# Performance work log

Hardware: AMD Instinct MI355X
Metric: run time of the kernel (lower is better)

Reference implementation:

```python
import jax, jax.numpy as jnp
import numpy as np

B, T, K, DH = 64, 1024, 8, 256
H = 2 * DH  # gru hidden_size = 512


def setup_inputs() -> dict:
    key = jax.random.key(0)
    ks = jax.random.split(key, 8)
    scale = 1.0 / np.sqrt(H)
    return {
        "s": jax.random.normal(ks[0], (B, T, 1, DH), dtype=jnp.float32),
        "p": jax.random.normal(ks[1], (B, T, K, DH), dtype=jnp.float32),
        "W_ih": jax.random.uniform(ks[2], (3 * H, H), jnp.float32, -scale, scale),
        "W_hh": jax.random.uniform(ks[3], (3 * H, H), jnp.float32, -scale, scale),
        "b_ih": jax.random.uniform(ks[4], (3 * H,), jnp.float32, -scale, scale),
        "b_hh": jax.random.uniform(ks[5], (3 * H,), jnp.float32, -scale, scale),
        "W_t": jax.random.uniform(ks[6], (1, H), jnp.float32, -scale, scale),
        "b_t": jax.random.uniform(ks[7], (1,), jnp.float32, -scale, scale),
    }


def reference(s, p, W_ih, W_hh, b_ih, b_hh, W_t, b_t):
    # p is summed over its multi-hot dim, then concatenated with s -> GRU input.
    x = jnp.concatenate([s[:, :, 0, :], p.sum(axis=2)], axis=-1)  # [B, T, H]
    x = jnp.swapaxes(x, 0, 1)  # [T, B, H] (scan over time)
    # Precompute all input-side gate pre-activations in one big GEMM.
    gi = jnp.einsum("tbh,gh->tbg", x, W_ih) + b_ih  # [T, B, 3H]
    h0 = jnp.zeros((B, H), dtype=x.dtype)  # hidden reset per example (initHidden)

    def step(h, gi_t):
        gh = h @ W_hh.T + b_hh  # [B, 3H]
        i_r, i_z, i_n = jnp.split(gi_t, 3, axis=-1)
        h_r, h_z, h_n = jnp.split(gh, 3, axis=-1)
        r = jax.nn.sigmoid(i_r + h_r)
        z = jax.nn.sigmoid(i_z + h_z)
        n = jnp.tanh(i_n + r * h_n)
        h_new = (1.0 - z) * n + z * h
        return h_new, h_new

    _, hs = jax.lax.scan(step, h0, gi)  # hs: [T, B, H]
    # reward = sigmoid(Linear(hidden)) at every timestep
    rewards = jax.nn.sigmoid(jnp.einsum("tbh,oh->tbo", hs, W_t) + b_t)  # [T, B, 1]
    return jnp.swapaxes(rewards[..., 0], 0, 1)  # [B, T]
```

## Files before the change

kernel.cpp:

```cpp
#include <hip/hip_runtime.h>
#include <hip/hip_fp16.h>
#include <stdint.h>

#define TT 1024
#define BB 64
#define DHH 256
#define HH 512
#define G3 1536
#define CHK 256

typedef _Float16 f16;
typedef _Float16 f16x4 __attribute__((ext_vector_type(4)));
typedef _Float16 f16x8 __attribute__((ext_vector_type(8)));
typedef float f32x4 __attribute__((ext_vector_type(4)));
typedef unsigned long long u64;

__device__ __forceinline__ float sigm(float x){ return 1.0f/(1.0f+__expf(-x)); }
__device__ __forceinline__ float tanh_f(float x){ return 2.0f/(1.0f+__expf(-2.0f*x)) - 1.0f; }

__global__ void k_prep(const float* __restrict__ wih, const float* __restrict__ whh,
                       const float* __restrict__ bih, const float* __restrict__ bhh,
                       f16* __restrict__ wih_h, f16* __restrict__ whh_h, float* __restrict__ biasf){
  int i = blockIdx.x*256 + threadIdx.x;
  if (i < G3*HH){ wih_h[i] = (f16)wih[i]; whh_h[i] = (f16)whh[i]; }
  if (i < G3) biasf[i] = bih[i] + (i < 2*HH ? bhh[i] : 0.0f);
}

__global__ void k_buildx(const float* __restrict__ s, const float* __restrict__ p, f16* __restrict__ x){
  int m = blockIdx.x;
  int t = m >> 6, b = m & 63;
  int l = threadIdx.x;
  const float4* s4 = reinterpret_cast<const float4*>(s + ((size_t)b*TT + t)*DHH);
  const float4* p4 = reinterpret_cast<const float4*>(p + ((size_t)b*TT + t)*8*DHH);
  float4 sv = s4[l];
  float4 a  = p4[l];
#pragma unroll
  for (int k=1;k<8;k++){ float4 v = p4[k*64 + l]; a.x+=v.x; a.y+=v.y; a.z+=v.z; a.w+=v.w; }
  f16* xr = x + (size_t)m*HH;
  f16x4 hs = { (f16)sv.x,(f16)sv.y,(f16)sv.z,(f16)sv.w };
  f16x4 hp = { (f16)a.x,(f16)a.y,(f16)a.z,(f16)a.w };
  *reinterpret_cast<f16x4*>(xr + l*4)       = hs;
  *reinterpret_cast<f16x4*>(xr + 256 + l*4) = hp;
}

#define LDAP 72
__global__ __launch_bounds__(256) void k_gemm(const f16* __restrict__ x, const f16* __restrict__ w,
                       const float* __restrict__ biasf, f16* __restrict__ gi){
  __shared__ f16 lA[128*LDAP];
  __shared__ f16 lB[128*LDAP];
  int by = blockIdx.x;
  int bx = blockIdx.y;
  int tid = threadIdx.x, l = tid & 63, wv = tid >> 6;
  int wm = wv >> 1, wn = wv & 1;

  f32x4 acc[4][4];
#pragma unroll
  for (int i=0;i<4;i++)
#pragma unroll
    for (int j=0;j<4;j++) acc[i][j] = (f32x4){0.f,0.f,0.f,0.f};

  for (int kt = 0; kt < 8; ++kt){
#pragma unroll
    for (int r = 0; r < 4; ++r){
      int c = tid + 256*r;
      int row = c >> 3, o = c & 7;
      f16x8 va = *reinterpret_cast<const f16x8*>(w + (size_t)(by*128+row)*HH + kt*64 + o*8);
      f16x8 vb = *reinterpret_cast<const f16x8*>(x + (size_t)(bx*128+row)*HH + kt*64 + o*8);
      *reinterpret_cast<f16x8*>(&lA[row*LDAP + o*8]) = va;
      *reinterpret_cast<f16x8*>(&lB[row*LDAP + o*8]) = vb;
    }
    __syncthreads();
#pragma unroll
    for (int kk = 0; kk < 2; ++kk){
      f16x8 aF[4], bF[4];
#pragma unroll
      for (int mi=0;mi<4;mi++)
        aF[mi] = *reinterpret_cast<const f16x8*>(&lA[(wm*64+mi*16+(l&15))*LDAP + kk*32 + (l>>4)*8]);
#pragma unroll
      for (int ni=0;ni<4;ni++)
        bF[ni] = *reinterpret_cast<const f16x8*>(&lB[(wn*64+ni*16+(l&15))*LDAP + kk*32 + (l>>4)*8]);
#pragma unroll
      for (int mi=0;mi<4;mi++)
#pragma unroll
        for (int ni=0;ni<4;ni++)
          acc[mi][ni] = __builtin_amdgcn_mfma_f32_16x16x32_f16(aF[mi], bF[ni], acc[mi][ni], 0,0,0);
    }
    __syncthreads();
  }
#pragma unroll
  for (int mi=0;mi<4;mi++){
    int wrow0 = by*128 + wm*64 + mi*16 + (l>>4)*4;
    float4 bv = *reinterpret_cast<const float4*>(biasf + wrow0);
    int gate = wrow0 >> 9, j = wrow0 & 511, ksl = j >> 5, rp = gate*32 + (j&31);
#pragma unroll
    for (int ni=0;ni<4;ni++){
      int xrow = bx*128 + wn*64 + ni*16 + (l&15);
      int t = xrow >> 6, g = (xrow>>4)&3, bp = xrow & 15;
      size_t dst = ((((size_t)t*16 + ksl)*4 + g)*16 + bp)*96 + rp;
      union { u64 u; f16x4 h; } cv;
      cv.h = (f16x4){ (f16)(acc[mi][ni][0]+bv.x), (f16)(acc[mi][ni][1]+bv.y),
                      (f16)(acc[mi][ni][2]+bv.z), (f16)(acc[mi][ni][3]+bv.w) };
      *reinterpret_cast<u64*>(gi + dst) = cv.u;
    }
  }
}

__global__ __launch_bounds__(256, 1) void k_scan(const f16* __restrict__ whh_h, const f16* __restrict__ gi,
                      const float* __restrict__ bhh, f16* __restrict__ hh){
  __shared__ f16 hbF[2][16][64][8];
  const int bid = blockIdx.x;
  const int g = bid & 3, c = bid >> 2;
  const int tid = threadIdx.x;
  const int w = tid >> 6, l = tid & 63;
  const int lm = l & 15, lh = l >> 4;
  const int jsl = c*4 + w;

  f16x8 aW[3][16];
#pragma unroll
  for (int gate = 0; gate < 3; ++gate){
    const f16* wr = whh_h + ((size_t)gate*512 + jsl*16 + lm)*HH + lh*8;
#pragma unroll
    for (int kt = 0; kt < 16; ++kt)
      aW[gate][kt] = *reinterpret_cast<const f16x8*>(wr + kt*32);
  }
#pragma unroll
  for (int gate = 0; gate < 3; ++gate)
#pragma unroll
    for (int kt = 0; kt < 16; ++kt)
      asm volatile("" : "+a"(aW[gate][kt]));

  const int jglob = jsl*16 + lh*4;
  float4 bnv = *reinterpret_cast<const float4*>(bhh + 2*HH + jglob);
  float bna[4] = {bnv.x, bnv.y, bnv.z, bnv.w};
  const int ksl2 = jsl >> 1, jo = (jsl & 1)*16 + lh*4;

  union U64H { u64 u; f16x4 h; };
  U64H cA[3], cB[3], cC[3], ho, hn;
  ho.u = 0ull;

  {
    const f16* g0 = gi + ((((size_t)0*16 + ksl2)*4 + g)*16 + lm)*96;
    cA[0].u = *reinterpret_cast<const u64*>(g0 + jo);
    cA[1].u = *reinterpret_cast<const u64*>(g0 + 32 + jo);
    cA[2].u = *reinterpret_cast<const u64*>(g0 + 64 + jo);
    const f16* g1 = gi + ((((size_t)1*16 + ksl2)*4 + g)*16 + lm)*96;
    cB[0].u = *reinterpret_cast<const u64*>(g1 + jo);
    cB[1].u = *reinterpret_cast<const u64*>(g1 + 32 + jo);
    cB[2].u = *reinterpret_cast<const u64*>(g1 + 64 + jo);
    const f16* g2 = gi + ((((size_t)2*16 + ksl2)*4 + g)*16 + lm)*96;
    cC[0].u = *reinterpret_cast<const u64*>(g2 + jo);
    cC[1].u = *reinterpret_cast<const u64*>(g2 + 32 + jo);
    cC[2].u = *reinterpret_cast<const u64*>(g2 + 64 + jo);
#pragma unroll
    for (int r = 0; r < 4; ++r){
      float rg = sigm((float)cA[0].h[r]);
      float zg = sigm((float)cA[1].h[r]);
      float ng = tanh_f((float)cA[2].h[r] + rg*bna[r]);
      hn.h[r] = (f16)((1.0f - zg)*ng);
    }
    ho.u = hn.u;
    __hip_atomic_store(reinterpret_cast<u64*>(hh + ((((size_t)0*4 + g)*32 + jsl)*CHK + lm*16 + lh*4)),
                       hn.u, __ATOMIC_RELAXED, __HIP_MEMORY_SCOPE_AGENT);
  }

#define BODY(T, CUR, NXT2)                                                                           \
  {                                                                                                  \
    const int t_ = (T);                                                                              \
    const int par = t_ & 1;                                                                          \
    const u64* hsrc = reinterpret_cast<const u64*>(                                                  \
        hh + (((size_t)(t_-1)*4 + g)*32 + w*8)*CHK) + l;          \
    u64 qq[8];                                                                                       \
    int ok;                                                                                          \
    do {                                                                                             \
      ok = 1;                                                                                        \
      _Pragma("unroll")                                                                              \
      for (int q = 0; q < 8; ++q){                                                                   \
        qq[q] = __hip_atomic_load(hsrc + (size_t)q*(CHK/4), __ATOMIC_RELAXED, __HIP_MEMORY_SCOPE_AGENT); \
        ok &= ((unsigned)qq[q] != 0xFFFFFFFFu);                                                      \
      }                                                                                              \
    } while (!__all(ok));                                                                            \
    _Pragma("unroll")                                                                                \
    for (int q = 0; q < 8; ++q){                                                                     \
      const int jj  = w*8 + q;                                                                       \
      const int ktq = jj >> 1;                                                                       \
      const int lhq = (jj & 1)*2 + ((l&3)>>1);                                                       \
      *reinterpret_cast<u64*>(&hbF[par][ktq][(l>>2) + 16*lhq][(l&1)*4]) = qq[q];                     \
    }                                                                                                \
    __syncthreads();                                                                                 \
    {                             \
      const int tn_ = (t_+2 < TT) ? t_+2 : TT-1;                                                     \
      const f16* gn = gi + ((((size_t)tn_*16 + ksl2)*4 + g)*16 + lm)*96;                             \
      NXT2[0].u = *reinterpret_cast<const u64*>(gn + jo);                                            \
      NXT2[1].u = *reinterpret_cast<const u64*>(gn + 32 + jo);                                       \
      NXT2[2].u = *reinterpret_cast<const u64*>(gn + 64 + jo);                                       \
    }                                                                                                \
    f32x4 aR = (f32x4){0.f,0.f,0.f,0.f};                                                             \
    f32x4 aZ = (f32x4){0.f,0.f,0.f,0.f};                                                             \
    f32x4 aN = (f32x4){0.f,0.f,0.f,0.f};                                                             \
    _Pragma("unroll")                                                                                \
    for (int kt = 0; kt < 16; ++kt){                                                                 \
      f16x8 bF = *reinterpret_cast<const f16x8*>(&hbF[par][kt][l][0]);                               \
      aR = __builtin_amdgcn_mfma_f32_16x16x32_f16(aW[0][kt], bF, aR, 0,0,0);                         \
      aZ = __builtin_amdgcn_mfma_f32_16x16x32_f16(aW[1][kt], bF, aZ, 0,0,0);                         \
      aN = __builtin_amdgcn_mfma_f32_16x16x32_f16(aW[2][kt], bF, aN, 0,0,0);                         \
    }                                                                                                \
    _Pragma("unroll")                                                                                \
    for (int r = 0; r < 4; ++r){                                                                     \
      float rg = sigm((float)CUR[0].h[r] + aR[r]);                                                   \
      float zg = sigm((float)CUR[1].h[r] + aZ[r]);                                                   \
      float ng = tanh_f((float)CUR[2].h[r] + rg*(aN[r] + bna[r]));                                   \
      hn.h[r] = (f16)((1.0f - zg)*ng + zg*(float)ho.h[r]);                                           \
    }                                                                                                \
    ho.u = hn.u;                                                                                     \
    __hip_atomic_store(reinterpret_cast<u64*>(hh + ((((size_t)t_*4 + g)*32 + jsl)*CHK + lm*16 + lh*4)),\
                       hn.u, __ATOMIC_RELAXED, __HIP_MEMORY_SCOPE_AGENT);                            \
  }

  for (int t = 1; t < TT; t += 3){
    BODY(t,   cB, cA)
    BODY(t+1, cC, cB)
    BODY(t+2, cA, cC)
  }
#undef BODY
}

__global__ void k_reward(const f16* __restrict__ hh, const float* __restrict__ wt,
                         const float* __restrict__ bt, float* __restrict__ out){
  int wv = threadIdx.x >> 6, l = threadIdx.x & 63;
  int idx = blockIdx.x*4 + wv;
  int b = idx >> 10, t = idx & 1023;
  int g = b >> 4, bl = b & 15;
  const f16* hr = hh + (((size_t)t*4 + g)*32 + (l >> 1))*CHK + bl*16 + (l & 1)*8;
  f16x8 hv = *reinterpret_cast<const f16x8*>(hr);
  float4 w0 = *reinterpret_cast<const float4*>(wt + l*8);
  float4 w1 = *reinterpret_cast<const float4*>(wt + l*8 + 4);
  float sum = (float)hv[0]*w0.x + (float)hv[1]*w0.y + (float)hv[2]*w0.z + (float)hv[3]*w0.w
            + (float)hv[4]*w1.x + (float)hv[5]*w1.y + (float)hv[6]*w1.z + (float)hv[7]*w1.w;
#pragma unroll
  for (int m=32;m>=1;m>>=1) sum += __shfl_xor(sum, m);
  if (l==0) out[idx] = sigm(sum + bt[0]);
}

extern "C" void kernel_launch(void* const* d_in, const int* in_sizes, int n_in,
                              void* d_out, int out_size, void* d_ws, size_t ws_size,
                              hipStream_t stream) {
  const float* s   = (const float*)d_in[0];
  const float* p   = (const float*)d_in[1];
  const float* wih = (const float*)d_in[2];
  const float* whh = (const float*)d_in[3];
  const float* bih = (const float*)d_in[4];
  const float* bhh = (const float*)d_in[5];
  const float* wt  = (const float*)d_in[6];
  const float* bt  = (const float*)d_in[7];
  float* out = (float*)d_out;

  char* ws = (char*)d_ws;
  size_t o = 0;
  auto take = [&](size_t bytes)->char*{ char* r = ws + o; o = (o + bytes + 255) & ~(size_t)255; return r; };
  f16*      x_h   = (f16*)   take((size_t)TT*BB*HH*2);
  f16*      wih_h = (f16*)   take((size_t)G3*HH*2);
  f16*      whh_h = (f16*)   take((size_t)G3*HH*2);
  float*    biasf = (float*) take((size_t)G3*4);
  f16*      gi_s  = (f16*)   take((size_t)TT*BB*G3*2);
  f16*      hh    = (f16*)   take((size_t)TT*BB*HH*2);
  (void)ws_size; (void)in_sizes; (void)n_in; (void)out_size;

  hipMemsetAsync(hh, 0xFF, (size_t)TT*BB*HH*2, stream);
  k_prep  <<<3072, 256, 0, stream>>>(wih, whh, bih, bhh, wih_h, whh_h, biasf);
  k_buildx<<<TT*BB, 64, 0, stream>>>(s, p, x_h);
  k_gemm  <<<dim3(12, 512), 256, 0, stream>>>(x_h, wih_h, biasf, gi_s);
  k_scan  <<<32, 256, 0, stream>>>(whh_h, gi_s, bhh, hh);
  k_reward<<<TT*BB/4, 256, 0, stream>>>(hh, wt, bt, out);
}
```

Before: 2.872 ms.

## Add sc0 fast-path polling buffer with MALL fallback and spread scan blocks

Each hidden-state chunk is now published to two buffers: a fast copy written with sc0 stores, which reuses the x_h workspace, and the original agent-scope atomic copy. Consumers first poll the fast copy a bounded number of times using sc0 loads, then fall back to spinning on the atomic copy. The scan grid doubles to 64 blocks, and half of them exit at once, which changes which CUs or XCDs the working blocks land on. The aim is lower cross-block handoff latency per timestep, at the cost of an extra memset and extra stores. If the fast copy is not coherent across XCDs, the fast path may rarely succeed.

```diff
diff --git a/kernel.cpp b/kernel.cpp
--- a/kernel.cpp
+++ b/kernel.cpp
@@ -8,6 +8,7 @@
 #define HH 512
 #define G3 1536
 #define CHK 256
+#define KF 6
 
 typedef _Float16 f16;
 typedef _Float16 f16x4 __attribute__((ext_vector_type(4)));
@@ -106,10 +107,11 @@
 }
 
 __global__ __launch_bounds__(256, 1) void k_scan(const f16* __restrict__ whh_h, const f16* __restrict__ gi,
-                      const float* __restrict__ bhh, f16* __restrict__ hh){
+                      const float* __restrict__ bhh, f16* __restrict__ hfast, f16* __restrict__ hmall){
   __shared__ f16 hbF[2][16][64][8];
   const int bid = blockIdx.x;
-  const int g = bid & 3, c = bid >> 2;
+  if ((bid & 7) >= 4) return;
+  const int g = bid & 7, c = bid >> 3;
   const int tid = threadIdx.x;
   const int w = tid >> 6, l = tid & 63;
   const int lm = l & 15, lh = l >> 4;
@@ -129,14 +131,22 @@
     for (int kt = 0; kt < 16; ++kt)
       asm volatile("" : "+a"(aW[gate][kt]));
 
-  const int jglob = jsl*16 + lh*4;
-  float4 bnv = *reinterpret_cast<const float4*>(bhh + 2*HH + jglob);
+  float4 bnv = *reinterpret_cast<const float4*>(bhh + 2*HH + jsl*16 + lh*4);
   float bna[4] = {bnv.x, bnv.y, bnv.z, bnv.w};
   const int ksl2 = jsl >> 1, jo = (jsl & 1)*16 + lh*4;
 
   union U64H { u64 u; f16x4 h; };
   U64H cA[3], cB[3], cC[3], ho, hn;
   ho.u = 0ull;
+
+  const size_t pofs = (size_t)lm*16 + lh*4;
+  auto publish = [&](int t, u64 v){
+    const size_t cbase = (((size_t)t*4 + g)*32 + jsl)*CHK + pofs;
+    f16* fd = hfast + cbase;
+    asm volatile("global_store_dwordx2 %0, %1, off sc0" :: "v"(fd), "v"(v) : "memory");
+    __hip_atomic_store(reinterpret_cast<u64*>(hmall + cbase), v,
+                       __ATOMIC_RELAXED, __HIP_MEMORY_SCOPE_AGENT);
+  };
 
   {
     const f16* g0 = gi + ((((size_t)0*16 + ksl2)*4 + g)*16 + lm)*96;
@@ -159,26 +169,54 @@
       hn.h[r] = (f16)((1.0f - zg)*ng);
     }
     ho.u = hn.u;
-    __hip_atomic_store(reinterpret_cast<u64*>(hh + ((((size_t)0*4 + g)*32 + jsl)*CHK + lm*16 + lh*4)),
-                       hn.u, __ATOMIC_RELAXED, __HIP_MEMORY_SCOPE_AGENT);
+    publish(0, hn.u);
   }
 
 #define BODY(T, CUR, NXT2)                                                                           \
   {                                                                                                  \
     const int t_ = (T);                                                                              \
     const int par = t_ & 1;                                                                          \
-    const u64* hsrc = reinterpret_cast<const u64*>(                                                  \
-        hh + (((size_t)(t_-1)*4 + g)*32 + w*8)*CHK) + l;          \
+    const size_t pollbase = (((size_t)(t_-1)*4 + g)*32 + w*8)*CHK;             \
     u64 qq[8];                                                                                       \
-    int ok;                                                                                          \
-    do {                                                                                             \
-      ok = 1;                                                                                        \
-      _Pragma("unroll")                                                                              \
-      for (int q = 0; q < 8; ++q){                                                                   \
-        qq[q] = __hip_atomic_load(hsrc + (size_t)q*(CHK/4), __ATOMIC_RELAXED, __HIP_MEMORY_SCOPE_AGENT); \
-        ok &= ((unsigned)qq[q] != 0xFFFFFFFFu);                                                      \
+    int got = 0;                                                                                     \
+    {                                                                                                \
+      const char* fb = reinterpret_cast<const char*>(hfast + pollbase) + (size_t)l*8;                \
+      for (int att = 0; att < KF && !got; ++att){                                                    \
+        u64 ff0,ff1,ff2,ff3,ff4,ff5,ff6,ff7;                                                         \
+        asm volatile(                                                                                \
+          "global_load_dwordx2 %0, %8, off sc0\n\t"                                                  \
+          "global_load_dwordx2 %1, %8, off offset:512 sc0\n\t"                                       \
+          "global_load_dwordx2 %2, %8, off offset:1024 sc0\n\t"                                      \
+          "global_load_dwordx2 %3, %8, off offset:1536 sc0\n\t"                                      \
+          "global_load_dwordx2 %4, %8, off offset:2048 sc0\n\t"                                      \
+          "global_load_dwordx2 %5, %8, off offset:2560 sc0\n\t"                                      \
+          "global_load_dwordx2 %6, %8, off offset:3072 sc0\n\t"                                      \
+          "global_load_dwordx2 %7, %8, off offset:3584 sc0\n\t"                                      \
+          "s_waitcnt vmcnt(0)"                                                                       \
+          : "=&v"(ff0),"=&v"(ff1),"=&v"(ff2),"=&v"(ff3),                                             \
+            "=&v"(ff4),"=&v"(ff5),"=&v"(ff6),"=&v"(ff7)                                              \
+          : "v"(fb) : "memory");                                                                     \
+        int ok = (int)((unsigned)ff0 != 0xFFFFFFFFu) & (int)((unsigned)ff1 != 0xFFFFFFFFu)           \
+               & (int)((unsigned)ff2 != 0xFFFFFFFFu) & (int)((unsigned)ff3 != 0xFFFFFFFFu)           \
+               & (int)((unsigned)ff4 != 0xFFFFFFFFu) & (int)((unsigned)ff5 != 0xFFFFFFFFu)           \
+               & (int)((unsigned)ff6 != 0xFFFFFFFFu) & (int)((unsigned)ff7 != 0xFFFFFFFFu);          \
+        got = __all(ok);                                                                             \
+        if (got){ qq[0]=ff0; qq[1]=ff1; qq[2]=ff2; qq[3]=ff3;                                        \
+                  qq[4]=ff4; qq[5]=ff5; qq[6]=ff6; qq[7]=ff7; }                                      \
       }                                                                                              \
-    } while (!__all(ok));                                                                            \
+    }                                                                                                \
+    if (!got){                                                                                       \
+      const u64* hsrc = reinterpret_cast<const u64*>(hmall + pollbase) + l;                          \
+      int ok;                                                                                        \
+      do {                                                                                           \
+        ok = 1;                                                                                      \
+        _Pragma("unroll")                                                                            \
+        for (int q = 0; q < 8; ++q){                                                                 \
+          qq[q] = __hip_atomic_load(hsrc + (size_t)q*(CHK/4), __ATOMIC_RELAXED, __HIP_MEMORY_SCOPE_AGENT); \
+          ok &= ((unsigned)qq[q] != 0xFFFFFFFFu);                                                    \
+        }                                                                                            \
+      } while (!__all(ok));                                                                          \
+    }                                                                                                \
     _Pragma("unroll")                                                                                \
     for (int q = 0; q < 8; ++q){                                                                     \
       const int jj  = w*8 + q;                                                                       \
@@ -187,7 +225,7 @@
       *reinterpret_cast<u64*>(&hbF[par][ktq][(l>>2) + 16*lhq][(l&1)*4]) = qq[q];                     \
     }                                                                                                \
     __syncthreads();                                                                                 \
-    {                             \
+    {                                                  \
       const int tn_ = (t_+2 < TT) ? t_+2 : TT-1;                                                     \
       const f16* gn = gi + ((((size_t)tn_*16 + ksl2)*4 + g)*16 + lm)*96;                             \
       NXT2[0].u = *reinterpret_cast<const u64*>(gn + jo);                                            \
@@ -212,8 +250,7 @@
       hn.h[r] = (f16)((1.0f - zg)*ng + zg*(float)ho.h[r]);                                           \
     }                                                                                                \
     ho.u = hn.u;                                                                                     \
-    __hip_atomic_store(reinterpret_cast<u64*>(hh + ((((size_t)t_*4 + g)*32 + jsl)*CHK + lm*16 + lh*4)),\
-                       hn.u, __ATOMIC_RELAXED, __HIP_MEMORY_SCOPE_AGENT);                            \
+    publish(t_, hn.u);                                                                               \
   }
 
   for (int t = 1; t < TT; t += 3){
@@ -262,13 +299,15 @@
   f16*      whh_h = (f16*)   take((size_t)G3*HH*2);
   float*    biasf = (float*) take((size_t)G3*4);
   f16*      gi_s  = (f16*)   take((size_t)TT*BB*G3*2);
-  f16*      hh    = (f16*)   take((size_t)TT*BB*HH*2);
+  f16*      hmall = (f16*)   take((size_t)TT*BB*HH*2);
+  f16*      hfast = x_h;
   (void)ws_size; (void)in_sizes; (void)n_in; (void)out_size;
 
-  hipMemsetAsync(hh, 0xFF, (size_t)TT*BB*HH*2, stream);
+  hipMemsetAsync(hmall, 0xFF, (size_t)TT*BB*HH*2, stream);
   k_prep  <<<3072, 256, 0, stream>>>(wih, whh, bih, bhh, wih_h, whh_h, biasf);
   k_buildx<<<TT*BB, 64, 0, stream>>>(s, p, x_h);
   k_gemm  <<<dim3(12, 512), 256, 0, stream>>>(x_h, wih_h, biasf, gi_s);
-  k_scan  <<<32, 256, 0, stream>>>(whh_h, gi_s, bhh, hh);
-  k_reward<<<TT*BB/4, 256, 0, stream>>>(hh, wt, bt, out);
-}
+  hipMemsetAsync(hfast, 0xFF, (size_t)TT*BB*HH*2, stream);
+  k_scan  <<<64, 256, 0, stream>>>(whh_h, gi_s, bhh, hfast, hmall);
+  k_reward<<<TT*BB/4, 256, 0, stream>>>(hmall, wt, bt, out);
+}
```

Result: slower. 3.244 ms (+13.0%).
